# Kernel optimization log

Hardware: AMD Instinct MI355X
Metric: run time of the kernel (lower is better)

## Reference

```python
import jax, jax.numpy as jnp
import numpy as np

N = 50000      # nodes
E = 800000     # directed edges
IN = 64        # in_dim
ED = 16        # edge_dim
H = 8          # heads
D = 32         # hdim (per-head out channels)
NM = 500       # molecules (graphs)
SLOPE = 0.2    # GATConv negative_slope
MLP_SLOPE = 0.01  # torch LeakyReLU default in the Sequential


def _glorot(k, shape, fan_in):
    return jax.random.normal(k, shape, jnp.float32) * (1.0 / np.sqrt(fan_in))


def setup_inputs() -> dict:
    key = jax.random.key(0)
    ks = jax.random.split(key, 32)
    inp = {}
    inp["x"] = jax.random.normal(ks[0], (N, IN), jnp.float32)
    inp["edge_index"] = jax.random.randint(ks[1], (2, E), 0, N)
    inp["edge_attr"] = jax.random.normal(ks[2], (E, ED), jnp.float32)
    inp["batch"] = jnp.sort(jax.random.randint(ks[3], (N,), 0, NM))
    ins = [IN, H * D, H * D]
    i = 4
    for l in range(3):
        inp[f"W{l+1}"] = _glorot(ks[i], (ins[l], H * D), ins[l]); i += 1
        inp[f"as{l+1}"] = _glorot(ks[i], (H, D), D); i += 1
        inp[f"ad{l+1}"] = _glorot(ks[i], (H, D), D); i += 1
        inp[f"We{l+1}"] = _glorot(ks[i], (ED, H * D), ED); i += 1
        inp[f"ae{l+1}"] = _glorot(ks[i], (H, D), D); i += 1
        inp[f"b{l+1}"] = jnp.zeros((H * D,), jnp.float32); i += 1
    # final MLP: 4*H*D -> 3*D -> 2*D -> 1
    inp["lw1"] = _glorot(ks[i], (4 * H * D, 3 * D), 4 * H * D); i += 1
    inp["lb1"] = jnp.zeros((3 * D,), jnp.float32)
    inp["lw2"] = _glorot(ks[i], (3 * D, 2 * D), 3 * D); i += 1
    inp["lb2"] = jnp.zeros((2 * D,), jnp.float32)
    inp["lw3"] = _glorot(ks[i], (2 * D, 1), 2 * D); i += 1
    inp["lb3"] = jnp.zeros((1,), jnp.float32)
    return inp


def _gat_conv(x, src, dst, ea, W, a_s, a_d, We, a_e, b):
    n = x.shape[0]
    xl = (x @ W).reshape(n, H, D)           # [N,H,D]
    el = (ea @ We).reshape(-1, H, D)        # [E',H,D]
    a_src = jnp.einsum('nhd,hd->nh', xl, a_s)
    a_dst = jnp.einsum('nhd,hd->nh', xl, a_d)
    a_edg = jnp.einsum('ehd,hd->eh', el, a_e)
    alpha = a_src[src] + a_dst[dst] + a_edg         # [E',H]
    alpha = jax.nn.leaky_relu(alpha, SLOPE)
    amax = jax.ops.segment_max(alpha, dst, num_segments=n)
    ex = jnp.exp(alpha - amax[dst])
    den = jax.ops.segment_sum(ex, dst, num_segments=n)
    att = ex / den[dst]                              # segment softmax over dst
    msg = xl[src] * att[:, :, None]                  # [E',H,D]
    out = jax.ops.segment_sum(msg, dst, num_segments=n)
    return out.reshape(n, H * D) + b


def reference(x, edge_index, edge_attr, batch,
              W1, as1, ad1, We1, ae1, b1,
              W2, as2, ad2, We2, ae2, b2,
              W3, as3, ad3, We3, ae3, b3,
              lw1, lb1, lw2, lb2, lw3, lb3):
    n = x.shape[0]
    src0, dst0 = edge_index[0], edge_index[1]
    loop = jnp.arange(n)
    src = jnp.concatenate([src0, loop])
    dst = jnp.concatenate([dst0, loop])
    # fill_value='add': self-loop edge_attr = sum of incoming edge_attr per node
    ea_loop = jax.ops.segment_sum(edge_attr, dst0, num_segments=n)
    ea = jnp.concatenate([edge_attr, ea_loop], axis=0)

    h1 = _gat_conv(x, src, dst, ea, W1, as1, ad1, We1, ae1, b1)
    h2 = _gat_conv(h1, src, dst, ea, W2, as2, ad2, We2, ae2, b2)
    h3 = _gat_conv(h2, src, dst, ea, W3, as3, ad3, We3, ae3, b3)

    h_pool = jax.ops.segment_sum(h3, batch, num_segments=NM)
    h_pool_ = h_pool[batch]   # == repeat_interleave(h_pool, counts) for sorted batch
    h = jnp.concatenate([h1, h2, h3, h_pool_], axis=1)
    h = jax.nn.leaky_relu(h @ lw1 + lb1, MLP_SLOPE)
    h = jax.nn.leaky_relu(h @ lw2 + lb2, MLP_SLOPE)
    h = h @ lw3 + lb3
    return jax.nn.sigmoid(h)
```

## Files before the change

kernel.cpp:

```cpp
#include <hip/hip_runtime.h>
#include <hip/hip_bf16.h>

namespace {
constexpr int kN    = 50000;
constexpr int kE    = 800000;
constexpr int kEtot = kE + kN;
constexpr int kEd   = 16;
constexpr int kH    = 8;
constexpr int kD    = 32;
constexpr int kC    = kH * kD;
constexpr int kNM   = 500;
constexpr int kNB   = (kN + 255) / 256;
constexpr int kCap  = 128;
}

typedef __attribute__((ext_vector_type(8))) _Float16 half8;
typedef __attribute__((ext_vector_type(4))) float floatx4;

__device__ __forceinline__ float h2f(ushort u) {
  union { ushort u; _Float16 h; } v;
  v.u = u;
  return (float)v.h;
}
__device__ __forceinline__ ushort f2h(float f) {
  union { _Float16 h; ushort u; } v;
  v.h = (_Float16)f;
  return v.u;
}

__global__ void gat_zero2(int* __restrict__ a, int* __restrict__ b, int n) {
  int i = blockIdx.x * blockDim.x + threadIdx.x;
  if (i < n) { a[i] = 0; b[i] = 0; }
}

__global__ void gat_zeropad(ushort* __restrict__ c1h) {
  int i = blockIdx.x * blockDim.x + threadIdx.x;
  if (i >= kN * 4) return;
  int row = i >> 2, q = i & 3;
  uint4 z = {0u, 0u, 0u, 0u};
  *(uint4*)(c1h + (long)row * 128 + 96 + q * 8) = z;
}

__global__ void cvt_all(const float* __restrict__ x,
                        const float* __restrict__ W1, const float* __restrict__ W2,
                        const float* __restrict__ W3, const float* __restrict__ lw1,
                        const float* __restrict__ lw2,
                        ushort* __restrict__ xh, ushort* __restrict__ Wt1,
                        ushort* __restrict__ Wt2, ushort* __restrict__ Wt3,
                        ushort* __restrict__ lwt1, ushort* __restrict__ lwt2p) {
  int i = blockIdx.x * blockDim.x + threadIdx.x;
  if (i < kN * 64) { xh[i] = f2h(x[i]); return; }
  i -= kN * 64;
  if (i < 256 * 64) {
    int n = i >> 6, k = i & 63;
    Wt1[i] = f2h(W1[(long)k * 256 + n]);
    return;
  }
  i -= 256 * 64;
  if (i < 256 * 256) {
    int n = i >> 8, k = i & 255;
    Wt2[i] = f2h(W2[(long)k * 256 + n]);
    return;
  }
  i -= 256 * 256;
  if (i < 256 * 256) {
    int n = i >> 8, k = i & 255;
    Wt3[i] = f2h(W3[(long)k * 256 + n]);
    return;
  }
  i -= 256 * 256;
  if (i < 96 * 1024) {
    int n = i >> 10, k = i & 1023;
    lwt1[i] = f2h(lw1[(long)k * 96 + n]);
    return;
  }
  i -= 96 * 1024;
  if (i < 64 * 128) {
    int n = i >> 7, k = i & 127;
    lwt2p[i] = (k < 96) ? f2h(lw2[(long)k * 64 + n]) : (ushort)0;
    return;
  }
}

__global__ void gat_make_q3(const float* __restrict__ We1, const float* __restrict__ ae1,
                            const float* __restrict__ We2, const float* __restrict__ ae2,
                            const float* __restrict__ We3, const float* __restrict__ ae3,
                            float* __restrict__ Q3) {
  int t = threadIdx.x;
  if (t >= 384) return;
  int l = t >> 7, r = t & 127;
  const float* We = (l == 0) ? We1 : (l == 1) ? We2 : We3;
  const float* ae = (l == 0) ? ae1 : (l == 1) ? ae2 : ae3;
  int c = r >> 3, h = r & 7;
  float s = 0.f;
#pragma unroll
  for (int d = 0; d < kD; d++) s += We[c * kC + h * kD + d] * ae[h * kD + d];
  Q3[l * 128 + c * kH + h] = s;
}

__global__ void gat_count(const int* __restrict__ ei, int* __restrict__ deg) {
  int e = blockIdx.x * blockDim.x + threadIdx.x;
  if (e >= kE) return;
  atomicAdd(&deg[ei[kE + e]], 1);
}

__global__ __launch_bounds__(256) void gat_scan_a(const int* __restrict__ deg,
                                                  int* __restrict__ offs,
                                                  int* __restrict__ bsum) {
  __shared__ int s[256];
  int b = blockIdx.x, t = threadIdx.x;
  int i = b * 256 + t;
  int v = (i < kN) ? deg[i] + 1 : 0;
  s[t] = v;
  __syncthreads();
  for (int o = 1; o < 256; o <<= 1) {
    int u = (t >= o) ? s[t - o] : 0;
    __syncthreads();
    s[t] += u;
    __syncthreads();
  }
  if (i < kN) offs[i] = s[t] - v;
  if (t == 255) bsum[b] = s[255];
}

__global__ __launch_bounds__(256) void gat_scan_b(const int* __restrict__ bsum,
                                                  int* __restrict__ bpre) {
  __shared__ int s[256];
  int t = threadIdx.x;
  int v = (t < kNB) ? bsum[t] : 0;
  s[t] = v;
  __syncthreads();
  for (int o = 1; o < 256; o <<= 1) {
    int u = (t >= o) ? s[t - o] : 0;
    __syncthreads();
    s[t] += u;
    __syncthreads();
  }
  if (t < kNB) bpre[t] = s[t] - v;
}

__global__ void gat_scan_c(int* __restrict__ offs, const int* __restrict__ bpre) {
  int i = blockIdx.x * blockDim.x + threadIdx.x;
  if (i < kN) offs[i] += bpre[blockIdx.x];
  if (i == 0) offs[kN] = kEtot;
}

__global__ void gat_fill(const int* __restrict__ ei, const int* __restrict__ offs,
                         int* __restrict__ fillc, int* __restrict__ el,
                         int* __restrict__ esrc, int* __restrict__ epos) {
  int e = blockIdx.x * blockDim.x + threadIdx.x;
  if (e >= kEtot) return;
  int s, d;
  if (e < kE) { s = ei[e]; d = ei[kE + e]; }
  else { s = d = e - kE; }
  int pos = offs[d] + atomicAdd(&fillc[d], 1);
  el[pos] = e;
  esrc[pos] = s;
  epos[e] = pos;
}

__global__ __launch_bounds__(256) void gat_aq(const int* __restrict__ el,
                                              const float* __restrict__ ea,
                                              const float* __restrict__ Q3,
                                              ushort* __restrict__ aq0,
                                              ushort* __restrict__ aq1,
                                              ushort* __restrict__ aq2) {
  __shared__ float Qs[384];
  int t = threadIdx.x;
  for (int i = t; i < 384; i += 256) Qs[i] = Q3[i];
  __syncthreads();
  int pos = blockIdx.x * blockDim.x + t;
  if (pos >= kEtot) return;
  int e = el[pos];
  long base = (long)pos * kH;
  if (e >= kE) {
    uint4 z = {0u, 0u, 0u, 0u};
    *(uint4*)(aq0 + base) = z;
    *(uint4*)(aq1 + base) = z;
    *(uint4*)(aq2 + base) = z;
    return;
  }
  float eav[kEd];
#pragma unroll
  for (int q = 0; q < kEd / 4; q++) {
    float4 v = *(const float4*)(ea + (long)e * kEd + q * 4);
    eav[q * 4 + 0] = v.x; eav[q * 4 + 1] = v.y;
    eav[q * 4 + 2] = v.z; eav[q * 4 + 3] = v.w;
  }
  ushort* outp[3] = {aq0, aq1, aq2};
#pragma unroll
  for (int l = 0; l < 3; l++) {
    union { uint4 u; ushort us[8]; } o;
#pragma unroll
    for (int h = 0; h < kH; h++) {
      float q = 0.f;
#pragma unroll
      for (int c = 0; c < kEd; c++) q += eav[c] * Qs[l * 128 + c * kH + h];
      o.us[h] = f2h(q);
    }
    *(uint4*)(outp[l] + base) = o.u;
  }
}

__global__ void gat_aqsum(const int* __restrict__ offs, const int* __restrict__ epos,
                          ushort* __restrict__ aq0, ushort* __restrict__ aq1,
                          ushort* __restrict__ aq2) {
  int t = blockIdx.x * blockDim.x + threadIdx.x;
  if (t >= kN * kH) return;
  int n = t >> 3, h = t & 7;
  int lo = offs[n], hi = offs[n + 1];
  float s0 = 0.f, s1 = 0.f, s2 = 0.f;
  for (int j = lo; j < hi; j++) {
    s0 += h2f(aq0[(long)j * kH + h]);
    s1 += h2f(aq1[(long)j * kH + h]);
    s2 += h2f(aq2[(long)j * kH + h]);
  }
  long sp = (long)epos[kE + n] * kH + h;
  aq0[sp] = f2h(s0);
  aq1[sp] = f2h(s1);
  aq2[sp] = f2h(s2);
}

template <int AMODE, int COEF>
__global__ __launch_bounds__(256) void gat_gemm_mfma(
    int M, int K, int N,
    const ushort* __restrict__ A0, const ushort* __restrict__ A1,
    const ushort* __restrict__ A2, const ushort* __restrict__ A3,
    const int* __restrict__ batch,
    const ushort* __restrict__ Bt, const float* __restrict__ bias,
    float* __restrict__ C, int ldc, ushort* __restrict__ Ch, int ldch, int act,
    const float* __restrict__ as_, const float* __restrict__ ad_,
    float* __restrict__ a_src, float* __restrict__ a_dst) {
  __shared__ ushort As[8][64][8];
  __shared__ ushort Bs[8][128][8];
  int t = threadIdx.x;
  int rowBase = blockIdx.y * 64;
  int colBase = blockIdx.x * 128;
  int w = t >> 6, L = t & 63;

  floatx4 acc[8];
#pragma unroll
  for (int i = 0; i < 8; i++) acc[i] = (floatx4){0.f, 0.f, 0.f, 0.f};

  int ar = t >> 2, akq = t & 3;
  int arow = rowBase + ar;
  int bn = t >> 1, bq2 = (t & 1) * 4;
  int bok = (colBase + bn) < N;
  long brow = (long)(colBase + bn) * K;

  for (int k0 = 0; k0 < K; k0 += 64) {
#pragma unroll
    for (int half = 0; half < 2; half++) {
      int q = akq + half * 4;
      int gk = k0 + q * 8;
      uint4 av = {0u, 0u, 0u, 0u};
      if (arow < M) {
        if (AMODE == 0) {
          av = *(const uint4*)(A0 + (long)arow * K + gk);
        } else {
          int j = gk >> 8, kc = gk & 255;
          const ushort* src = (j == 0) ? A0 : (j == 1) ? A1 : (j == 2) ? A2 : A3;
          long rr = (j == 3) ? (long)batch[arow] : (long)arow;
          av = *(const uint4*)(src + rr * 256 + kc);
        }
      }
      *(uint4*)&As[q][ar][0] = av;
    }
#pragma unroll
    for (int u = 0; u < 4; u++) {
      int q = bq2 + u;
      uint4 bv = {0u, 0u, 0u, 0u};
      if (bok) bv = *(const uint4*)(Bt + brow + k0 + q * 8);
      *(uint4*)&Bs[q][bn][0] = bv;
    }
    __syncthreads();
    int mrow = w * 16 + (L & 15);
    int nl = L & 15;
#pragma unroll
    for (int half = 0; half < 2; half++) {
      int q = (L >> 4) + half * 4;
      half8 af = *(const half8*)&As[q][mrow][0];
#pragma unroll
      for (int t8 = 0; t8 < 8; t8++) {
        half8 bf = *(const half8*)&Bs[q][t8 * 16 + nl][0];
        acc[t8] = __builtin_amdgcn_mfma_f32_16x16x32_f16(af, bf, acc[t8], 0, 0, 0);
      }
    }
    __syncthreads();
  }
  int nlo = L & 15;
  int rbase = rowBase + w * 16 + (L >> 4) * 4;
#pragma unroll
  for (int t8 = 0; t8 < 8; t8++) {
    int col = colBase + t8 * 16 + nlo;
    if (col >= N) continue;
    float bv = bias ? bias[col] : 0.f;
#pragma unroll
    for (int r = 0; r < 4; r++) {
      int row = rbase + r;
      if (row >= M) continue;
      float v = acc[t8][r] + bv;
      if (act == 1) v = v > 0.f ? v : 0.01f * v;
      if (C) C[(long)row * ldc + col] = v;
      if (Ch) Ch[(long)row * ldch + col] = f2h(v);
    }
  }
  if (COEF) {
    float ps[4][4], pd[4][4];
#pragma unroll
    for (int g = 0; g < 4; g++)
#pragma unroll
      for (int r = 0; r < 4; r++) { ps[g][r] = 0.f; pd[g][r] = 0.f; }
    int hA = colBase >> 5;
#pragma unroll
    for (int t8 = 0; t8 < 8; t8++) {
      int g = t8 >> 1;
      int widx = (t8 & 1) * 16 + nlo;
      float wsv = as_[(hA + g) * kD + widx];
      float wdv = ad_[(hA + g) * kD + widx];
#pragma unroll
      for (int r = 0; r < 4; r++) {
        ps[g][r] += acc[t8][r] * wsv;
        pd[g][r] += acc[t8][r] * wdv;
      }
    }
#pragma unroll
    for (int m = 1; m < 16; m <<= 1) {
#pragma unroll
      for (int g = 0; g < 4; g++)
#pragma unroll
        for (int r = 0; r < 4; r++) {
          ps[g][r] += __shfl_xor(ps[g][r], m);
          pd[g][r] += __shfl_xor(pd[g][r], m);
        }
    }
    if (nlo == 0) {
#pragma unroll
      for (int r = 0; r < 4; r++) {
        int row = rbase + r;
        if (row >= M) continue;
#pragma unroll
        for (int g = 0; g < 4; g++) {
          a_src[row * kH + hA + g] = ps[g][r];
          a_dst[row * kH + hA + g] = pd[g][r];
        }
      }
    }
  }
}

__global__ __launch_bounds__(256, 8) void gat_aggregate(
    const int* __restrict__ offs, const int* __restrict__ esrc,
    const ushort* __restrict__ aq,
    const float* __restrict__ a_src, const float* __restrict__ a_dst,
    const ushort* __restrict__ xlh, const float* __restrict__ bias,
    ushort* __restrict__ hh) {
  __shared__ float alf[4][kCap][kH];
  __shared__ int srcs[4][kCap];
  int wid = threadIdx.x >> 6;
  int n = blockIdx.x * 4 + wid;
  int L = threadIdx.x & 63;
  int lo = offs[n], hi = offs[n + 1];
  int deg = hi - lo;
  bool fits = (deg <= kCap);
  int hp = L & 7, sl = L >> 3;
  float adr = a_dst[n * kH + hp];
  float m = -1e30f;
  if (fits) {
    for (int j = lo + sl; j < hi; j += 8) {
      int sidx = esrc[j];
      float a = a_src[sidx * kH + hp] + adr + h2f(aq[(long)j * kH + hp]);
      a = a > 0.f ? a : 0.2f * a;
      alf[wid][j - lo][hp] = a;
      if (hp == 0) srcs[wid][j - lo] = sidx;
      m = fmaxf(m, a);
    }
  } else {
    for (int j = lo + sl; j < hi; j += 8) {
      float a = a_src[esrc[j] * kH + hp] + adr + h2f(aq[(long)j * kH + hp]);
      a = a > 0.f ? a : 0.2f * a;
      m = fmaxf(m, a);
    }
  }
#pragma unroll
  for (int msk = 8; msk < 64; msk <<= 1) m = fmaxf(m, __shfl_xor(m, msk));
  __syncthreads();
  float s = 0.f;
  if (fits) {
    for (int j = lo + sl; j < hi; j += 8) {
      float pp = __expf(alf[wid][j - lo][hp] - m);
      alf[wid][j - lo][hp] = pp;
      s += pp;
    }
  } else {
    for (int j = lo + sl; j < hi; j += 8) {
      float a = a_src[esrc[j] * kH + hp] + adr + h2f(aq[(long)j * kH + hp]);
      a = a > 0.f ? a : 0.2f * a;
      s += __expf(a - m);
    }
  }
#pragma unroll
  for (int msk = 8; msk < 64; msk <<= 1) s += __shfl_xor(s, msk);
  __syncthreads();
  int eh = L >> 5;
  int cl = L & 31;
  int c = cl * 8;
  int h = cl >> 2;
  float invs = 1.f / __shfl(s, h);
  float mh = __shfl(m, h);
  float acc[8] = {0.f, 0.f, 0.f, 0.f, 0.f, 0.f, 0.f, 0.f};
  union { uint4 u; _Float16 hf[8]; } v0, v1, v2, v3;
  if (fits) {
    int j = lo;
    for (; j + 8 <= hi; j += 8) {
      int j0 = j + eh, j1 = j + 2 + eh, j2 = j + 4 + eh, j3 = j + 6 + eh;
      int s0 = srcs[wid][j0 - lo];
      int s1 = srcs[wid][j1 - lo];
      int s2 = srcs[wid][j2 - lo];
      int s3 = srcs[wid][j3 - lo];
      float t0 = alf[wid][j0 - lo][h];
      float t1 = alf[wid][j1 - lo][h];
      float t2 = alf[wid][j2 - lo][h];
      float t3 = alf[wid][j3 - lo][h];
      v0.u = *(const uint4*)(xlh + (long)s0 * kC + c);
      v1.u = *(const uint4*)(xlh + (long)s1 * kC + c);
      v2.u = *(const uint4*)(xlh + (long)s2 * kC + c);
      v3.u = *(const uint4*)(xlh + (long)s3 * kC + c);
#pragma unroll
      for (int i = 0; i < 8; i++) acc[i] += t0 * (float)v0.hf[i];
#pragma unroll
      for (int i = 0; i < 8; i++) acc[i] += t1 * (float)v1.hf[i];
#pragma unroll
      for (int i = 0; i < 8; i++) acc[i] += t2 * (float)v2.hf[i];
#pragma unroll
      for (int i = 0; i < 8; i++) acc[i] += t3 * (float)v3.hf[i];
    }
    for (; j < hi; j += 2) {
      int jj = j + eh;
      bool valid = jj < hi;
      int idx = valid ? jj - lo : 0;
      int sn = srcs[wid][idx];
      float att = valid ? alf[wid][idx][h] : 0.f;
      v0.u = *(const uint4*)(xlh + (long)sn * kC + c);
#pragma unroll
      for (int i = 0; i < 8; i++) acc[i] += att * (float)v0.hf[i];
    }
  } else {
    float adh = a_dst[n * kH + h];
    for (int j = lo; j < hi; j += 2) {
      int jj = j + eh;
      bool valid = jj < hi;
      int js = valid ? jj : lo;
      int sn = esrc[js];
      float a = a_src[sn * kH + h] + adh + h2f(aq[(long)js * kH + h]);
      a = a > 0.f ? a : 0.2f * a;
      float att = valid ? __expf(a - mh) : 0.f;
      v0.u = *(const uint4*)(xlh + (long)sn * kC + c);
#pragma unroll
      for (int i = 0; i < 8; i++) acc[i] += att * (float)v0.hf[i];
    }
  }
#pragma unroll
  for (int i = 0; i < 8; i++) acc[i] += __shfl_xor(acc[i], 32);
  if (eh == 0) {
    float4 b0 = *(const float4*)(bias + c);
    float4 b1 = *(const float4*)(bias + c + 4);
    ushort o[8];
    o[0] = f2h(acc[0] * invs + b0.x); o[1] = f2h(acc[1] * invs + b0.y);
    o[2] = f2h(acc[2] * invs + b0.z); o[3] = f2h(acc[3] * invs + b0.w);
    o[4] = f2h(acc[4] * invs + b1.x); o[5] = f2h(acc[5] * invs + b1.y);
    o[6] = f2h(acc[6] * invs + b1.z); o[7] = f2h(acc[7] * invs + b1.w);
    *(uint4*)(hh + (long)n * kC + c) = *(uint4*)o;
  }
}

__global__ __launch_bounds__(256) void gat_pool_seg(const ushort* __restrict__ h3h,
                                                    const int* __restrict__ batch,
                                                    ushort* __restrict__ hpoolh) {
  int m = blockIdx.x;
  int c = threadIdx.x;
  int lo = 0, hi = kN;
  while (lo < hi) { int mid = (lo + hi) >> 1; if (batch[mid] < m) lo = mid + 1; else hi = mid; }
  int start = lo;
  hi = kN;
  while (lo < hi) { int mid = (lo + hi) >> 1; if (batch[mid] < m + 1) lo = mid + 1; else hi = mid; }
  int end = lo;
  float s = 0.f;
  for (int n = start; n < end; n++) s += h2f(h3h[(long)n * kC + c]);
  hpoolh[(long)m * kC + c] = f2h(s);
}

__global__ void gat_mlp3(const float* __restrict__ c2, const float* __restrict__ lw3,
                         const float* __restrict__ lb3, float* __restrict__ out) {
  int n = blockIdx.x * blockDim.x + threadIdx.x;
  if (n >= kN) return;
  float s = lb3[0];
  const float* r = c2 + (long)n * 64;
#pragma unroll
  for (int k = 0; k < 64; k++) s += r[k] * lw3[k];
  float v = 1.f / (1.f + __expf(-s));
  out[n] = v;
}

static inline int cdiv(int a, int b) { return (a + b - 1) / b; }

extern "C" void kernel_launch(void* const* d_in, const int* in_sizes, int n_in,
                              void* d_out, int out_size, void* d_ws, size_t ws_size,
                              hipStream_t stream) {
  (void)in_sizes; (void)n_in; (void)out_size; (void)ws_size;
  const float* x = (const float*)d_in[0];
  const int* ei = (const int*)d_in[1];
  const float* ea = (const float*)d_in[2];
  const int* batch = (const int*)d_in[3];
  const float *W[3], *as_[3], *ad_[3], *We_[3], *ae_[3], *bb[3];
  for (int l = 0; l < 3; l++) {
    W[l]   = (const float*)d_in[4 + 6 * l];
    as_[l] = (const float*)d_in[5 + 6 * l];
    ad_[l] = (const float*)d_in[6 + 6 * l];
    We_[l] = (const float*)d_in[7 + 6 * l];
    ae_[l] = (const float*)d_in[8 + 6 * l];
    bb[l]  = (const float*)d_in[9 + 6 * l];
  }
  const float* lw1 = (const float*)d_in[22];
  const float* lb1 = (const float*)d_in[23];
  const float* lw2 = (const float*)d_in[24];
  const float* lb2 = (const float*)d_in[25];
  const float* lw3 = (const float*)d_in[26];
  const float* lb3 = (const float*)d_in[27];
  float* out = (float*)d_out;

  char* p = (char*)d_ws;
  auto carve = [&](size_t bytes) -> void* {
    void* r = (void*)p;
    p += (bytes + 255) & ~(size_t)255;
    return r;
  };
  ushort* aq0    = (ushort*)carve(sizeof(ushort) * (size_t)kEtot * kH);
  ushort* aq1    = (ushort*)carve(sizeof(ushort) * (size_t)kEtot * kH);
  ushort* aq2    = (ushort*)carve(sizeof(ushort) * (size_t)kEtot * kH);
  float* a_src   = (float*)carve(sizeof(float) * (size_t)kN * kH);
  float* a_dst   = (float*)carve(sizeof(float) * (size_t)kN * kH);
  float* Q3      = (float*)carve(sizeof(float) * 3 * 128);
  float* c2      = (float*)carve(sizeof(float) * (size_t)kN * 64);
  ushort* xh     = (ushort*)carve(sizeof(ushort) * (size_t)kN * 64);
  ushort* xlh    = (ushort*)carve(sizeof(ushort) * (size_t)kN * kC);
  ushort* h1h    = (ushort*)carve(sizeof(ushort) * (size_t)kN * kC);
  ushort* h2h    = (ushort*)carve(sizeof(ushort) * (size_t)kN * kC);
  ushort* h3h    = (ushort*)carve(sizeof(ushort) * (size_t)kN * kC);
  ushort* hpoolh = (ushort*)carve(sizeof(ushort) * (size_t)kNM * kC);
  ushort* Wt1    = (ushort*)carve(sizeof(ushort) * 64 * 256);
  ushort* Wt2    = (ushort*)carve(sizeof(ushort) * 256 * 256);
  ushort* Wt3    = (ushort*)carve(sizeof(ushort) * 256 * 256);
  ushort* lwt1   = (ushort*)carve(sizeof(ushort) * 1024 * 96);
  ushort* lwt2p  = (ushort*)carve(sizeof(ushort) * 64 * 128);
  int* deg   = (int*)carve(sizeof(int) * kN);
  int* fillc = (int*)carve(sizeof(int) * kN);
  int* offs  = (int*)carve(sizeof(int) * (kN + 1));
  int* bsum  = (int*)carve(sizeof(int) * 256);
  int* bpre  = (int*)carve(sizeof(int) * 256);
  int* el    = (int*)carve(sizeof(int) * kEtot);
  int* esrc  = (int*)carve(sizeof(int) * kEtot);
  int* epos  = (int*)carve(sizeof(int) * kEtot);
  ushort* c1h = aq0;

  gat_zero2<<<cdiv(kN, 256), 256, 0, stream>>>(deg, fillc, kN);
  {
    int tot = kN * 64 + 256 * 64 + 2 * 256 * 256 + 96 * 1024 + 64 * 128;
    cvt_all<<<cdiv(tot, 256), 256, 0, stream>>>(x, W[0], W[1], W[2], lw1, lw2,
                                                xh, Wt1, Wt2, Wt3, lwt1, lwt2p);
  }
  gat_make_q3<<<1, 384, 0, stream>>>(We_[0], ae_[0], We_[1], ae_[1], We_[2], ae_[2], Q3);

  gat_count<<<cdiv(kE, 256), 256, 0, stream>>>(ei, deg);
  gat_scan_a<<<kNB, 256, 0, stream>>>(deg, offs, bsum);
  gat_scan_b<<<1, 256, 0, stream>>>(bsum, bpre);
  gat_scan_c<<<kNB, 256, 0, stream>>>(offs, bpre);
  gat_fill<<<cdiv(kEtot, 256), 256, 0, stream>>>(ei, offs, fillc, el, esrc, epos);
  gat_aq<<<cdiv(kEtot, 256), 256, 0, stream>>>(el, ea, Q3, aq0, aq1, aq2);
  gat_aqsum<<<cdiv(kN * kH, 256), 256, 0, stream>>>(offs, epos, aq0, aq1, aq2);

  const ushort* hinh[3] = {xh, h1h, h2h};
  ushort* houth[3] = {h1h, h2h, h3h};
  const ushort* Wt[3] = {Wt1, Wt2, Wt3};
  const ushort* aqP[3] = {aq0, aq1, aq2};
  int kdim[3] = {64, kC, kC};
  for (int l = 0; l < 3; l++) {
    dim3 ggrid(kC / 128, cdiv(kN, 64));
    gat_gemm_mfma<0, 1><<<ggrid, 256, 0, stream>>>(
        kN, kdim[l], kC, hinh[l], nullptr, nullptr, nullptr, nullptr,
        Wt[l], nullptr, nullptr, 0, xlh, kC, 0,
        as_[l], ad_[l], a_src, a_dst);
    gat_aggregate<<<kN / 4, 256, 0, stream>>>(offs, esrc, aqP[l], a_src, a_dst,
                                              xlh, bb[l], houth[l]);
  }

  gat_pool_seg<<<kNM, kC, 0, stream>>>(h3h, batch, hpoolh);

  {
    gat_zeropad<<<cdiv(kN * 4, 256), 256, 0, stream>>>(c1h);
    dim3 g1(1, cdiv(kN, 64));
    gat_gemm_mfma<2, 0><<<g1, 256, 0, stream>>>(
        kN, 4 * kC, 96, h1h, h2h, h3h, hpoolh, batch,
        lwt1, lb1, nullptr, 0, c1h, 128, 1,
        nullptr, nullptr, nullptr, nullptr);
    dim3 g2(1, cdiv(kN, 64));
    gat_gemm_mfma<0, 0><<<g2, 256, 0, stream>>>(
        kN, 128, 64, c1h, nullptr, nullptr, nullptr, nullptr,
        lwt2p, lb2, c2, 64, nullptr, 0, 1,
        nullptr, nullptr, nullptr, nullptr);
    gat_mlp3<<<cdiv(kN, 256), 256, 0, stream>>>(c2, lw3, lb3, out);
  }
}
```

Before: 717.1 us.

## Fuse setup kernels, compute self-loop attention in aggregate, fold final MLP layer into GEMM

Merges the zero, convert, Q3 and degree-count kernels into one launch, with hipMemsetAsync doing the zeroing. The separate aq self-loop summation pass is dropped: the aggregate kernel now accumulates incoming edge attention terms on the fly and substitutes the self-loop value itself. The final 64->1 layer and sigmoid are fused into the second MLP GEMM epilogue, which removes the c2 buffer. The zero-pad kernel is merged with pooling, and pooling gets 4-way unrolled accumulation. The intent is fewer launches and less memory traffic, at the cost of extra shuffles and branches in the aggregate kernel.

New measurement: 670.7 us. 1.07x faster.

```diff
diff --git a/kernel.cpp b/kernel.cpp
--- a/kernel.cpp
+++ b/kernel.cpp
@@ -28,26 +28,18 @@
   return v.u;
 }
 
-__global__ void gat_zero2(int* __restrict__ a, int* __restrict__ b, int n) {
-  int i = blockIdx.x * blockDim.x + threadIdx.x;
-  if (i < n) { a[i] = 0; b[i] = 0; }
-}
-
-__global__ void gat_zeropad(ushort* __restrict__ c1h) {
-  int i = blockIdx.x * blockDim.x + threadIdx.x;
-  if (i >= kN * 4) return;
-  int row = i >> 2, q = i & 3;
-  uint4 z = {0u, 0u, 0u, 0u};
-  *(uint4*)(c1h + (long)row * 128 + 96 + q * 8) = z;
-}
-
-__global__ void cvt_all(const float* __restrict__ x,
+__global__ void gat_pre(const float* __restrict__ x,
                         const float* __restrict__ W1, const float* __restrict__ W2,
                         const float* __restrict__ W3, const float* __restrict__ lw1,
                         const float* __restrict__ lw2,
                         ushort* __restrict__ xh, ushort* __restrict__ Wt1,
                         ushort* __restrict__ Wt2, ushort* __restrict__ Wt3,
-                        ushort* __restrict__ lwt1, ushort* __restrict__ lwt2p) {
+                        ushort* __restrict__ lwt1, ushort* __restrict__ lwt2p,
+                        const int* __restrict__ ei, int* __restrict__ deg,
+                        const float* __restrict__ We1, const float* __restrict__ ae1,
+                        const float* __restrict__ We2, const float* __restrict__ ae2,
+                        const float* __restrict__ We3, const float* __restrict__ ae3,
+                        float* __restrict__ Q3) {
   int i = blockIdx.x * blockDim.x + threadIdx.x;
   if (i < kN * 64) { xh[i] = f2h(x[i]); return; }
   i -= kN * 64;
@@ -80,28 +72,22 @@
     lwt2p[i] = (k < 96) ? f2h(lw2[(long)k * 64 + n]) : (ushort)0;
     return;
   }
-}
-
-__global__ void gat_make_q3(const float* __restrict__ We1, const float* __restrict__ ae1,
-                            const float* __restrict__ We2, const float* __restrict__ ae2,
-                            const float* __restrict__ We3, const float* __restrict__ ae3,
-                            float* __restrict__ Q3) {
-  int t = threadIdx.x;
-  if (t >= 384) return;
-  int l = t >> 7, r = t & 127;
-  const float* We = (l == 0) ? We1 : (l == 1) ? We2 : We3;
-  const float* ae = (l == 0) ? ae1 : (l == 1) ? ae2 : ae3;
-  int c = r >> 3, h = r & 7;
-  float s = 0.f;
-#pragma unroll
-  for (int d = 0; d < kD; d++) s += We[c * kC + h * kD + d] * ae[h * kD + d];
-  Q3[l * 128 + c * kH + h] = s;
-}
-
-__global__ void gat_count(const int* __restrict__ ei, int* __restrict__ deg) {
-  int e = blockIdx.x * blockDim.x + threadIdx.x;
-  if (e >= kE) return;
-  atomicAdd(&deg[ei[kE + e]], 1);
+  i -= 64 * 128;
+  if (i < kE) {
+    atomicAdd(&deg[ei[kE + i]], 1);
+    return;
+  }
+  i -= kE;
+  if (i < 384) {
+    int l = i >> 7, r = i & 127;
+    const float* We = (l == 0) ? We1 : (l == 1) ? We2 : We3;
+    const float* ae = (l == 0) ? ae1 : (l == 1) ? ae2 : ae3;
+    int c = r >> 3, h = r & 7;
+    float s = 0.f;
+#pragma unroll
+    for (int d = 0; d < kD; d++) s += We[c * kC + h * kD + d] * ae[h * kD + d];
+    Q3[l * 128 + c * kH + h] = s;
+  }
 }
 
 __global__ __launch_bounds__(256) void gat_scan_a(const int* __restrict__ deg,
@@ -202,25 +188,6 @@
   }
 }
 
-__global__ void gat_aqsum(const int* __restrict__ offs, const int* __restrict__ epos,
-                          ushort* __restrict__ aq0, ushort* __restrict__ aq1,
-                          ushort* __restrict__ aq2) {
-  int t = blockIdx.x * blockDim.x + threadIdx.x;
-  if (t >= kN * kH) return;
-  int n = t >> 3, h = t & 7;
-  int lo = offs[n], hi = offs[n + 1];
-  float s0 = 0.f, s1 = 0.f, s2 = 0.f;
-  for (int j = lo; j < hi; j++) {
-    s0 += h2f(aq0[(long)j * kH + h]);
-    s1 += h2f(aq1[(long)j * kH + h]);
-    s2 += h2f(aq2[(long)j * kH + h]);
-  }
-  long sp = (long)epos[kE + n] * kH + h;
-  aq0[sp] = f2h(s0);
-  aq1[sp] = f2h(s1);
-  aq2[sp] = f2h(s2);
-}
-
 template <int AMODE, int COEF>
 __global__ __launch_bounds__(256) void gat_gemm_mfma(
     int M, int K, int N,
@@ -230,7 +197,8 @@
     const ushort* __restrict__ Bt, const float* __restrict__ bias,
     float* __restrict__ C, int ldc, ushort* __restrict__ Ch, int ldch, int act,
     const float* __restrict__ as_, const float* __restrict__ ad_,
-    float* __restrict__ a_src, float* __restrict__ a_dst) {
+    float* __restrict__ a_src, float* __restrict__ a_dst,
+    const float* __restrict__ fw3, const float* __restrict__ fb3) {
   __shared__ ushort As[8][64][8];
   __shared__ ushort Bs[8][128][8];
   int t = threadIdx.x;
@@ -290,19 +258,48 @@
   }
   int nlo = L & 15;
   int rbase = rowBase + w * 16 + (L >> 4) * 4;
-#pragma unroll
-  for (int t8 = 0; t8 < 8; t8++) {
-    int col = colBase + t8 * 16 + nlo;
-    if (col >= N) continue;
-    float bv = bias ? bias[col] : 0.f;
-#pragma unroll
-    for (int r = 0; r < 4; r++) {
-      int row = rbase + r;
-      if (row >= M) continue;
-      float v = acc[t8][r] + bv;
-      if (act == 1) v = v > 0.f ? v : 0.01f * v;
-      if (C) C[(long)row * ldc + col] = v;
-      if (Ch) Ch[(long)row * ldch + col] = f2h(v);
+  if (act == 2) {
+    float dot[4] = {0.f, 0.f, 0.f, 0.f};
+#pragma unroll
+    for (int t8 = 0; t8 < 8; t8++) {
+      int col = colBase + t8 * 16 + nlo;
+      if (col >= N) continue;
+      float bv = bias[col];
+      float wv = fw3[col];
+#pragma unroll
+      for (int r = 0; r < 4; r++) {
+        float v = acc[t8][r] + bv;
+        v = v > 0.f ? v : 0.01f * v;
+        dot[r] += v * wv;
+      }
+    }
+#pragma unroll
+    for (int msk = 1; msk < 16; msk <<= 1)
+#pragma unroll
+      for (int r = 0; r < 4; r++) dot[r] += __shfl_xor(dot[r], msk);
+    if (nlo == 0) {
+      float b3 = fb3[0];
+#pragma unroll
+      for (int r = 0; r < 4; r++) {
+        int row = rbase + r;
+        if (row < M) C[row] = 1.f / (1.f + __expf(-(dot[r] + b3)));
+      }
+    }
+  } else {
+#pragma unroll
+    for (int t8 = 0; t8 < 8; t8++) {
+      int col = colBase + t8 * 16 + nlo;
+      if (col >= N) continue;
+      float bv = bias ? bias[col] : 0.f;
+#pragma unroll
+      for (int r = 0; r < 4; r++) {
+        int row = rbase + r;
+        if (row >= M) continue;
+        float v = acc[t8][r] + bv;
+        if (act == 1) v = v > 0.f ? v : 0.01f * v;
+        if (C) C[(long)row * ldc + col] = v;
+        if (Ch) Ch[(long)row * ldch + col] = f2h(v);
+      }
     }
   }
   if (COEF) {
@@ -351,6 +348,7 @@
 
 __global__ __launch_bounds__(256, 8) void gat_aggregate(
     const int* __restrict__ offs, const int* __restrict__ esrc,
+    const int* __restrict__ epos,
     const ushort* __restrict__ aq,
     const float* __restrict__ a_src, const float* __restrict__ a_dst,
     const ushort* __restrict__ xlh, const float* __restrict__ bias,
@@ -363,13 +361,17 @@
   int lo = offs[n], hi = offs[n + 1];
   int deg = hi - lo;
   bool fits = (deg <= kCap);
+  int spos = epos[kE + n];
   int hp = L & 7, sl = L >> 3;
   float adr = a_dst[n * kH + hp];
   float m = -1e30f;
+  float sq = 0.f;
   if (fits) {
     for (int j = lo + sl; j < hi; j += 8) {
       int sidx = esrc[j];
-      float a = a_src[sidx * kH + hp] + adr + h2f(aq[(long)j * kH + hp]);
+      float aqv = h2f(aq[(long)j * kH + hp]);
+      sq += aqv;
+      float a = a_src[sidx * kH + hp] + adr + aqv;
       a = a > 0.f ? a : 0.2f * a;
       alf[wid][j - lo][hp] = a;
       if (hp == 0) srcs[wid][j - lo] = sidx;
@@ -377,13 +379,22 @@
     }
   } else {
     for (int j = lo + sl; j < hi; j += 8) {
-      float a = a_src[esrc[j] * kH + hp] + adr + h2f(aq[(long)j * kH + hp]);
+      float aqv = h2f(aq[(long)j * kH + hp]);
+      sq += aqv;
+      float a = a_src[esrc[j] * kH + hp] + adr + aqv;
       a = a > 0.f ? a : 0.2f * a;
       m = fmaxf(m, a);
     }
   }
 #pragma unroll
-  for (int msk = 8; msk < 64; msk <<= 1) m = fmaxf(m, __shfl_xor(m, msk));
+  for (int msk = 8; msk < 64; msk <<= 1) {
+    m = fmaxf(m, __shfl_xor(m, msk));
+    sq += __shfl_xor(sq, msk);
+  }
+  float aself = a_src[n * kH + hp] + adr + sq;
+  aself = aself > 0.f ? aself : 0.2f * aself;
+  m = fmaxf(m, aself);
+  if (fits && sl == 0) alf[wid][spos - lo][hp] = aself;
   __syncthreads();
   float s = 0.f;
   if (fits) {
@@ -394,7 +405,8 @@
     }
   } else {
     for (int j = lo + sl; j < hi; j += 8) {
-      float a = a_src[esrc[j] * kH + hp] + adr + h2f(aq[(long)j * kH + hp]);
+      float aqv = (j == spos) ? sq : h2f(aq[(long)j * kH + hp]);
+      float a = a_src[esrc[j] * kH + hp] + adr + aqv;
       a = a > 0.f ? a : 0.2f * a;
       s += __expf(a - m);
     }
@@ -447,12 +459,14 @@
     }
   } else {
     float adh = a_dst[n * kH + h];
+    float sqh = __shfl(sq, h);
     for (int j = lo; j < hi; j += 2) {
       int jj = j + eh;
       bool valid = jj < hi;
       int js = valid ? jj : lo;
       int sn = esrc[js];
-      float a = a_src[sn * kH + h] + adh + h2f(aq[(long)js * kH + h]);
+      float aqv = (js == spos) ? sqh : h2f(aq[(long)js * kH + h]);
+      float a = a_src[sn * kH + h] + adh + aqv;
       a = a > 0.f ? a : 0.2f * a;
       float att = valid ? __expf(a - mh) : 0.f;
       v0.u = *(const uint4*)(xlh + (long)sn * kC + c);
@@ -474,9 +488,18 @@
   }
 }
 
-__global__ __launch_bounds__(256) void gat_pool_seg(const ushort* __restrict__ h3h,
+__global__ __launch_bounds__(256) void gat_pool_pad(const ushort* __restrict__ h3h,
                                                     const int* __restrict__ batch,
-                                                    ushort* __restrict__ hpoolh) {
+                                                    ushort* __restrict__ hpoolh,
+                                                    ushort* __restrict__ c1h) {
+  if (blockIdx.x >= kNM) {
+    int i = (blockIdx.x - kNM) * 256 + threadIdx.x;
+    if (i >= kN * 4) return;
+    int row = i >> 2, q = i & 3;
+    uint4 z = {0u, 0u, 0u, 0u};
+    *(uint4*)(c1h + (long)row * 128 + 96 + q * 8) = z;
+    return;
+  }
   int m = blockIdx.x;
   int c = threadIdx.x;
   int lo = 0, hi = kN;
@@ -485,21 +508,16 @@
   hi = kN;
   while (lo < hi) { int mid = (lo + hi) >> 1; if (batch[mid] < m + 1) lo = mid + 1; else hi = mid; }
   int end = lo;
-  float s = 0.f;
-  for (int n = start; n < end; n++) s += h2f(h3h[(long)n * kC + c]);
-  hpoolh[(long)m * kC + c] = f2h(s);
-}
-
-__global__ void gat_mlp3(const float* __restrict__ c2, const float* __restrict__ lw3,
-                         const float* __restrict__ lb3, float* __restrict__ out) {
-  int n = blockIdx.x * blockDim.x + threadIdx.x;
-  if (n >= kN) return;
-  float s = lb3[0];
-  const float* r = c2 + (long)n * 64;
-#pragma unroll
-  for (int k = 0; k < 64; k++) s += r[k] * lw3[k];
-  float v = 1.f / (1.f + __expf(-s));
-  out[n] = v;
+  float s0 = 0.f, s1 = 0.f, s2 = 0.f, s3 = 0.f;
+  int n = start;
+  for (; n + 4 <= end; n += 4) {
+    s0 += h2f(h3h[(long)n * kC + c]);
+    s1 += h2f(h3h[(long)(n + 1) * kC + c]);
+    s2 += h2f(h3h[(long)(n + 2) * kC + c]);
+    s3 += h2f(h3h[(long)(n + 3) * kC + c]);
+  }
+  for (; n < end; n++) s0 += h2f(h3h[(long)n * kC + c]);
+  hpoolh[(long)m * kC + c] = f2h((s0 + s1) + (s2 + s3));
 }
 
 static inline int cdiv(int a, int b) { return (a + b - 1) / b; }
@@ -541,7 +559,6 @@
   float* a_src   = (float*)carve(sizeof(float) * (size_t)kN * kH);
   float* a_dst   = (float*)carve(sizeof(float) * (size_t)kN * kH);
   float* Q3      = (float*)carve(sizeof(float) * 3 * 128);
-  float* c2      = (float*)carve(sizeof(float) * (size_t)kN * 64);
   ushort* xh     = (ushort*)carve(sizeof(ushort) * (size_t)kN * 64);
   ushort* xlh    = (ushort*)carve(sizeof(ushort) * (size_t)kN * kC);
   ushort* h1h    = (ushort*)carve(sizeof(ushort) * (size_t)kN * kC);
@@ -563,21 +580,20 @@
   int* epos  = (int*)carve(sizeof(int) * kEtot);
   ushort* c1h = aq0;
 
-  gat_zero2<<<cdiv(kN, 256), 256, 0, stream>>>(deg, fillc, kN);
+  hipMemsetAsync(deg, 0, sizeof(int) * kN, stream);
+  hipMemsetAsync(fillc, 0, sizeof(int) * kN, stream);
   {
-    int tot = kN * 64 + 256 * 64 + 2 * 256 * 256 + 96 * 1024 + 64 * 128;
-    cvt_all<<<cdiv(tot, 256), 256, 0, stream>>>(x, W[0], W[1], W[2], lw1, lw2,
-                                                xh, Wt1, Wt2, Wt3, lwt1, lwt2p);
-  }
-  gat_make_q3<<<1, 384, 0, stream>>>(We_[0], ae_[0], We_[1], ae_[1], We_[2], ae_[2], Q3);
-
-  gat_count<<<cdiv(kE, 256), 256, 0, stream>>>(ei, deg);
+    int tot = kN * 64 + 256 * 64 + 2 * 256 * 256 + 96 * 1024 + 64 * 128 + kE + 384;
+    gat_pre<<<cdiv(tot, 256), 256, 0, stream>>>(
+        x, W[0], W[1], W[2], lw1, lw2, xh, Wt1, Wt2, Wt3, lwt1, lwt2p,
+        ei, deg, We_[0], ae_[0], We_[1], ae_[1], We_[2], ae_[2], Q3);
+  }
+
   gat_scan_a<<<kNB, 256, 0, stream>>>(deg, offs, bsum);
   gat_scan_b<<<1, 256, 0, stream>>>(bsum, bpre);
   gat_scan_c<<<kNB, 256, 0, stream>>>(offs, bpre);
   gat_fill<<<cdiv(kEtot, 256), 256, 0, stream>>>(ei, offs, fillc, el, esrc, epos);
   gat_aq<<<cdiv(kEtot, 256), 256, 0, stream>>>(el, ea, Q3, aq0, aq1, aq2);
-  gat_aqsum<<<cdiv(kN * kH, 256), 256, 0, stream>>>(offs, epos, aq0, aq1, aq2);
 
   const ushort* hinh[3] = {xh, h1h, h2h};
   ushort* houth[3] = {h1h, h2h, h3h};
@@ -589,25 +605,23 @@
     gat_gemm_mfma<0, 1><<<ggrid, 256, 0, stream>>>(
         kN, kdim[l], kC, hinh[l], nullptr, nullptr, nullptr, nullptr,
         Wt[l], nullptr, nullptr, 0, xlh, kC, 0,
-        as_[l], ad_[l], a_src, a_dst);
-    gat_aggregate<<<kN / 4, 256, 0, stream>>>(offs, esrc, aqP[l], a_src, a_dst,
+        as_[l], ad_[l], a_src, a_dst, nullptr, nullptr);
+    gat_aggregate<<<kN / 4, 256, 0, stream>>>(offs, esrc, epos, aqP[l], a_src, a_dst,
                                               xlh, bb[l], houth[l]);
   }
 
-  gat_pool_seg<<<kNM, kC, 0, stream>>>(h3h, batch, hpoolh);
+  gat_pool_pad<<<kNM + cdiv(kN * 4, 256), 256, 0, stream>>>(h3h, batch, hpoolh, c1h);
 
   {
-    gat_zeropad<<<cdiv(kN * 4, 256), 256, 0, stream>>>(c1h);
     dim3 g1(1, cdiv(kN, 64));
     gat_gemm_mfma<2, 0><<<g1, 256, 0, stream>>>(
         kN, 4 * kC, 96, h1h, h2h, h3h, hpoolh, batch,
         lwt1, lb1, nullptr, 0, c1h, 128, 1,
-        nullptr, nullptr, nullptr, nullptr);
+        nullptr, nullptr, nullptr, nullptr, nullptr, nullptr);
     dim3 g2(1, cdiv(kN, 64));
     gat_gemm_mfma<0, 0><<<g2, 256, 0, stream>>>(
         kN, 128, 64, c1h, nullptr, nullptr, nullptr, nullptr,
-        lwt2p, lb2, c2, 64, nullptr, 0, 1,
-        nullptr, nullptr, nullptr, nullptr);
-    gat_mlp3<<<cdiv(kN, 256), 256, 0, stream>>>(c2, lw3, lb3, out);
-  }
-}
+        lwt2p, lb2, out, 1, nullptr, 0, 2,
+        nullptr, nullptr, nullptr, nullptr, lw3, lb3);
+  }
+}
```
